# Performance work log

Hardware: AMD Instinct MI355X
Metric: run time of the kernel (lower is better)

The kernel has to match this reference:

```python
import jax, jax.numpy as jnp
import numpy as np

A = 5            # num_anchors
NC = 20          # num_classes
IGNORE_THRESH = 0.6
COORD_SCALE = 1.0
NOOBJ_SCALE = 1.0
OBJ_SCALE = 5.0
CLASS_SCALE = 1.0
ANCHORS_NP = np.array([[0.052, 0.066], [0.14, 0.11], [0.24, 0.30], [0.45, 0.42], [0.77, 0.72]], dtype=np.float32)


def setup_inputs() -> dict:
    key = jax.random.key(0)
    k1, k2, k3, k4, k5 = jax.random.split(key, 5)
    B, F, O = 32, 38, 50
    C = A * (5 + NC)
    outputs = jax.random.normal(k1, (B, C, F, F), jnp.float32)
    # targets: (cx, cy, w, h, cls) normalized; padded rows are all-zero
    cxy = jax.random.uniform(k2, (B, O, 2), minval=0.15, maxval=0.85)
    wh = jax.random.uniform(k3, (B, O, 2), minval=0.05, maxval=0.20)
    cls = jax.random.randint(k4, (B, O), 0, NC).astype(jnp.float32)
    targets = jnp.concatenate([cxy, wh, cls[..., None]], axis=-1)
    nobj = jax.random.randint(k5, (B,), 10, O + 1)
    valid = (jnp.arange(O)[None, :] < nobj[:, None]).astype(jnp.float32)
    targets = targets * valid[..., None]
    return {"outputs": outputs, "targets": targets, "anchors": jnp.asarray(ANCHORS_NP)}


def _pairwise_iou_xywh(a, b):
    # a: (..., N, 4), b: (..., M, 4) center-format -> IoU (..., N, M)
    a = a[..., :, None, :]
    b = b[..., None, :, :]
    tl = jnp.maximum(a[..., :2] - a[..., 2:] * 0.5, b[..., :2] - b[..., 2:] * 0.5)
    br = jnp.minimum(a[..., :2] + a[..., 2:] * 0.5, b[..., :2] + b[..., 2:] * 0.5)
    wh = jnp.clip(br - tl, 0.0)
    inter = wh[..., 0] * wh[..., 1]
    area_a = a[..., 2] * a[..., 3]
    area_b = b[..., 2] * b[..., 3]
    return inter / (area_a + area_b - inter + 1e-12)


def _forward(outputs, targets, anchors):
    B, C, F, _ = outputs.shape
    S = F * F
    O = targets.shape[1]
    valid = targets.sum(axis=2) > 0                    # (B, O)
    gt = targets[..., :4] * F                          # grid-unit cxywh
    gt_cls = targets[..., 4]

    out5 = outputs.reshape(B, A, 5 + NC, F, F)
    jj = jnp.arange(F, dtype=outputs.dtype)            # x (last axis)
    ii = jnp.arange(F, dtype=outputs.dtype)[:, None]   # y
    aw = (anchors[:, 0] * F)[None, :, None, None]
    ah = (anchors[:, 1] * F)[None, :, None, None]
    px = jax.nn.sigmoid(out5[:, :, 0]) + jj
    py = jax.nn.sigmoid(out5[:, :, 1]) + ii
    pw = jnp.exp(out5[:, :, 2]) * aw
    ph = jnp.exp(out5[:, :, 3]) * ah
    pred_boxes = jnp.stack([px, py, pw, ph], -1).transpose(0, 2, 3, 1, 4).reshape(B, S * A, 4)

    # anchor prior boxes at cell centers: (S, A, 4)
    ax = jnp.broadcast_to(jj + 0.5, (F, F))
    ay = jnp.broadcast_to(ii + 0.5, (F, F))
    aa = jnp.stack([
        jnp.broadcast_to(ax[:, :, None], (F, F, A)),
        jnp.broadcast_to(ay[:, :, None], (F, F, A)),
        jnp.broadcast_to((anchors[:, 0] * F)[None, None, :], (F, F, A)),
        jnp.broadcast_to((anchors[:, 1] * F)[None, None, :], (F, F, A)),
    ], -1).reshape(S, A, 4)

    ious = _pairwise_iou_xywh(pred_boxes, gt)          # (B, S*A, O)
    ious = jnp.where(valid[:, None, :], ious, 0.0)     # padded objs excluded (IoU >= 0)
    max_iou = ious.reshape(B, S, A, O).max(axis=-1)    # (B, S, A)

    n_pos = jnp.any(max_iou > IGNORE_THRESH, axis=(1, 2))
    iou_mask = jnp.full((B, S, A), NOOBJ_SCALE, outputs.dtype)
    iou_mask = jnp.where(n_pos[:, None, None] & (max_iou >= IGNORE_THRESH), 0.0, iou_mask)

    overlaps = _pairwise_iou_xywh(aa.reshape(1, S * A, 4), gt).reshape(B, S, A, O)

    # responsible cell: floor of top-left corner (faithful to source), anchor = argmax prior overlap
    x1y1 = gt[..., :2] - gt[..., 2:] * 0.5
    cxcy = jnp.floor(x1y1).astype(jnp.int32)
    cell = jnp.clip(cxcy[..., 1] * F + cxcy[..., 0], 0, S - 1)             # (B, O)
    ovT = overlaps.transpose(0, 3, 1, 2)                                   # (B, O, S, A)
    ov_cell = jnp.take_along_axis(ovT, cell[:, :, None, None], axis=2)[:, :, 0, :]
    anchor_idx = jnp.argmax(ov_cell, axis=-1)                              # (B, O)
    resp = aa[cell, anchor_idx]                                            # (B, O, 4)
    deltas = jnp.stack([gt[..., 0] - resp[..., 0], gt[..., 1] - resp[..., 1],
                        gt[..., 2] / resp[..., 2], gt[..., 3] / resp[..., 3]], -1)
    mi = jnp.take_along_axis(jnp.take_along_axis(max_iou, cell[:, :, None], axis=1),
                             anchor_idx[:, :, None], axis=2)[..., 0]       # (B, O)

    b_rep = jnp.broadcast_to(jnp.arange(B)[:, None], (B, O))
    cell_s = jnp.where(valid, cell, S)  # OOB index for padded objs -> dropped
    zt = jnp.zeros((B, S, A), outputs.dtype)
    box_target = jnp.zeros((B, S, A, 4), outputs.dtype).at[b_rep, cell_s, anchor_idx].set(deltas, mode='drop')
    box_mask = zt.at[b_rep, cell_s, anchor_idx].set(1.0, mode='drop')
    class_target = zt.at[b_rep, cell_s, anchor_idx].set(gt_cls, mode='drop')
    class_mask = zt.at[b_rep, cell_s, anchor_idx].set(1.0, mode='drop')
    iou_target = zt.at[b_rep, cell_s, anchor_idx].set(mi, mode='drop')
    iou_mask = iou_mask.at[b_rep, cell_s, anchor_idx].set(OBJ_SCALE, mode='drop')

    # prediction side, layout (B, (i*F+j)*A + a, 5+NC) matching target layout
    outs = out5.transpose(0, 3, 4, 1, 2).reshape(B, S * A, 5 + NC)
    pd = jnp.concatenate([jax.nn.sigmoid(outs[..., :2]), jnp.exp(outs[..., 2:4])], -1)
    conf = jax.nn.sigmoid(outs[..., 4])
    probs = jax.nn.softmax(outs[..., 5:], axis=-1)

    bm = box_mask.reshape(B, S * A, 1)
    im = iou_mask.reshape(B, S * A)
    box_loss = jnp.sum((pd * bm - box_target.reshape(B, S * A, 4) * bm) ** 2)
    iou_loss = jnp.sum((conf * im - iou_target.reshape(B, S * A) * im) ** 2)
    # faithful quirk of the source: cross-entropy applied to softmax *outputs* as logits
    ls = jax.nn.log_softmax(probs, axis=-1)
    ct = class_target.reshape(B, S * A).astype(jnp.int32)
    ce = -jnp.take_along_axis(ls, ct[..., None], axis=-1)[..., 0]
    class_loss = jnp.sum(ce * class_mask.reshape(B, S * A))
    return (COORD_SCALE * box_loss + iou_loss + CLASS_SCALE * class_loss) / B


def reference(outputs, targets, anchors):
    return _forward(outputs, targets, anchors)
```

## Files before the change

### kernel.cpp

```cpp
#include <hip/hip_runtime.h>
#include <math.h>

#define A_N 5
#define NC 20
#define FD 38
#define SD (FD*FD)
#define BD 32
#define OD 50
#define SA (SD*A_N)
#define HALF (SA/2)
#define GXP 15
#define SLOTB 16
#define NSLOT (BD * SLOTB)
#define IGN_T 0.6f
#define OBJ_S 5.0f

__device__ __forceinline__ float sigm(float x) { return 1.0f / (1.0f + __expf(-x)); }

__global__ __launch_bounds__(256) void k_main(
    const float* __restrict__ outputs, const float* __restrict__ targets,
    const float* __restrict__ anchors,
    float* __restrict__ pbase, float* __restrict__ pcorr, int* __restrict__ pflag)
{
    __shared__ float4 g_box[OD];
    __shared__ float  g_e[OD];
    __shared__ float  s_anc[2 * A_N];
    __shared__ int    s_cnt, s_any;
    __shared__ int    s_key[OD];
    __shared__ float  wb[4], wc[4];

    const int b = blockIdx.y;
    const int tid = threadIdx.x;
    if (tid == 0) s_any = 0;
    if (tid < 2 * A_N) s_anc[tid] = anchors[tid];

    if (blockIdx.x == GXP) {
        if (tid == 0) s_cnt = 0;
        __syncthreads();
        float gx = 0, gy = 0, gw = 0, gh = 0;
        int ct = 0, key = -1;
        if (tid < OD) {
            const float* t = targets + (b * OD + tid) * 5;
            float tx = t[0], ty = t[1], tw = t[2], th = t[3], tc = t[4];
            if (tx + ty + tw + th + tc > 0.0f) {
                gx = tx * FD; gy = ty * FD; gw = tw * FD; gh = th * FD;
                float gtlx = gx - gw*0.5f, gtly = gy - gh*0.5f;
                float gbrx = gx + gw*0.5f, gbry = gy + gh*0.5f;
                int k = atomicAdd(&s_cnt, 1);
                g_box[k] = make_float4(gtlx, gtly, gbrx, gbry);
                g_e[k] = gw * gh + 1e-12f;
                int cx = (int)floorf(gtlx), cy = (int)floorf(gtly);
                int cell = min(max(cy * FD + cx, 0), SD - 1);
                int ci = cell / FD, cj = cell - ci * FD;
                float acx = (float)cj + 0.5f, acy = (float)ci + 0.5f;
                float areaB = gw * gh;
                float best = -1.0f; int bi = 0;
                for (int a = 0; a < A_N; ++a) {
                    float aw = s_anc[2*a] * FD, ah = s_anc[2*a+1] * FD;
                    float w = fmaxf(fminf(acx + aw*0.5f, gbrx) - fmaxf(acx - aw*0.5f, gtlx), 0.0f);
                    float h = fmaxf(fminf(acy + ah*0.5f, gbry) - fmaxf(acy - ah*0.5f, gtly), 0.0f);
                    float inter = w * h;
                    float iou = inter / (aw*ah + areaB - inter + 1e-12f);
                    if (iou > best) { best = iou; bi = a; }
                }
                key = bi * SD + cell;
                ct = (int)tc;
            }
        }
        if (tid < OD) s_key[tid] = key;
        __syncthreads();
        const int cnt = s_cnt;

        float rbase = 0.0f, rcorr = 0.0f;
        if (tid < OD && key >= 0) {
            int win = -1;
            #pragma unroll 10
            for (int o = 0; o < OD; ++o) win = (s_key[o] == key) ? o : win;
            if (win == tid) {
                int a = key / SD, cell = key - a * SD;
                int ci = cell / FD, cj = cell - ci * FD;
                const float* ob = outputs + ((size_t)b * (A_N * 25) + a * 25) * SD + cell;
                float o0 = ob[0], o1 = ob[SD], o2 = ob[2*SD], o3 = ob[3*SD], o4 = ob[4*SD];
                float aw = s_anc[2*a] * FD, ah = s_anc[2*a+1] * FD;
                float px = sigm(o0) + (float)cj;
                float py = sigm(o1) + (float)ci;
                float ew = __expf(o2), eh = __expf(o3);
                float pw = ew * aw, ph = eh * ah;
                float tlx = px - pw*0.5f, tly = py - ph*0.5f;
                float brx = px + pw*0.5f, bry = py + ph*0.5f;
                float ar = pw * ph;
                float bn = 0.0f, bd = 1.0f;
                for (int o = 0; o < cnt; ++o) {
                    float4 bx = g_box[o];
                    float w = fmaxf(fminf(brx, bx.z) - fmaxf(tlx, bx.x), 0.0f);
                    float h = fmaxf(fminf(bry, bx.w) - fmaxf(tly, bx.y), 0.0f);
                    float in = w * h, de = ar + g_e[o] - in;
                    if (in * bd > bn * de) { bn = in; bd = de; }
                }
                float mi = bn / bd;
                float conf = sigm(o4);
                float d = conf - mi;
                rbase += OBJ_S * OBJ_S * d * d;
                float c2 = conf * conf;
                if (bn >= IGN_T * bd) rcorr -= c2;
                else                  rbase -= c2;
                float dx = gx - ((float)cj + 0.5f);
                float dy = gy - ((float)ci + 0.5f);
                float e0 = sigm(o0) - dx;
                float e1 = sigm(o1) - dy;
                float e2 = ew - gw / aw;
                float e3 = eh - gh / ah;
                rbase += e0*e0 + e1*e1 + e2*e2 + e3*e3;
                const float* cb = ob + 5 * SD;
                float xmax = -INFINITY;
                #pragma unroll
                for (int k = 0; k < NC; ++k) xmax = fmaxf(xmax, cb[k * SD]);
                float esum = 0.0f;
                #pragma unroll
                for (int k = 0; k < NC; ++k) esum += __expf(cb[k * SD] - xmax);
                float inv = 1.0f / esum;
                float pmax = inv;
                float pct = __expf(cb[ct * SD] - xmax) * inv;
                float e2s = 0.0f;
                #pragma unroll
                for (int k = 0; k < NC; ++k)
                    e2s += __expf(__expf(cb[k * SD] - xmax) * inv - pmax);
                rbase += -(pct - (pmax + __logf(e2s)));
            }
        }
        #pragma unroll
        for (int off = 32; off > 0; off >>= 1) {
            rbase += __shfl_down(rbase, off);
            rcorr += __shfl_down(rcorr, off);
        }
        int lane = tid & 63, w = tid >> 6;
        if (lane == 0) { wb[w] = rbase; wc[w] = rcorr; }
        __syncthreads();
        if (tid == 0) {
            int gid = b * SLOTB + GXP;
            pbase[gid] = wb[0] + wb[1] + wb[2] + wb[3];
            pcorr[gid] = wc[0] + wc[1] + wc[2] + wc[3];
            pflag[gid] = 0;
        }
        return;
    }

    const int ix = blockIdx.x * 256 + tid;
    const bool act = (ix < HALF);
    const int p0 = ix, p1 = ix + HALF;
    int a0 = p0 / SD, r0 = p0 - a0 * SD;
    int a1 = p1 / SD, r1 = p1 - a1 * SD;
    int ii0 = r0 / FD, jj0 = r0 - ii0 * FD;
    int ii1 = r1 / FD, jj1 = r1 - ii1 * FD;
    const float* ob0 = outputs + ((size_t)b * (A_N * 25) + a0 * 25) * SD + r0;
    const float* ob1 = outputs + ((size_t)b * (A_N * 25) + a1 * 25) * SD + r1;
    float q00 = 0, q01 = 0, q02 = 0, q03 = 0, q04 = 0;
    float q10 = 0, q11 = 0, q12 = 0, q13 = 0, q14 = 0;
    if (act) {
        q00 = ob0[0]; q01 = ob0[SD]; q02 = ob0[2*SD]; q03 = ob0[3*SD]; q04 = ob0[4*SD];
        q10 = ob1[0]; q11 = ob1[SD]; q12 = ob1[2*SD]; q13 = ob1[3*SD]; q14 = ob1[4*SD];
    }

    if (tid < 64) {
        bool v = false;
        float gtlx = 0, gtly = 0, gbrx = 0, gbry = 0, e = 0;
        if (tid < OD) {
            const float* t = targets + (b * OD + tid) * 5;
            float tx = t[0], ty = t[1], tw = t[2], th = t[3], tc = t[4];
            if (tx + ty + tw + th + tc > 0.0f) {
                v = true;
                float gx = tx * FD, gy = ty * FD, gw = tw * FD, gh = th * FD;
                gtlx = gx - gw*0.5f; gtly = gy - gh*0.5f;
                gbrx = gx + gw*0.5f; gbry = gy + gh*0.5f;
                e = IGN_T * (gw * gh + 1e-12f);
            }
        }
        unsigned long long bal = __ballot(v);
        if (v) {
            int k = __popcll(bal & ((1ull << tid) - 1ull));
            g_box[k] = make_float4(gtlx, gtly, gbrx, gbry);
            g_e[k] = e;
        }
        if (tid == 0) s_cnt = __popcll(bal);
    }
    __syncthreads();
    const int cnt = s_cnt;

    float base = 0.0f, corr = 0.0f;
    bool hot = false;
    if (act) {
        float aw0 = s_anc[2*a0] * FD, ah0 = s_anc[2*a0+1] * FD;
        float aw1 = s_anc[2*a1] * FD, ah1 = s_anc[2*a1+1] * FD;
        float px0 = sigm(q00) + (float)jj0, py0 = sigm(q01) + (float)ii0;
        float px1 = sigm(q10) + (float)jj1, py1 = sigm(q11) + (float)ii1;
        float pw0 = __expf(q02) * aw0, ph0 = __expf(q03) * ah0;
        float pw1 = __expf(q12) * aw1, ph1 = __expf(q13) * ah1;
        float tlx0 = px0 - pw0*0.5f, tly0 = py0 - ph0*0.5f;
        float brx0 = px0 + pw0*0.5f, bry0 = py0 + ph0*0.5f;
        float tlx1 = px1 - pw1*0.5f, tly1 = py1 - ph1*0.5f;
        float brx1 = px1 + pw1*0.5f, bry1 = py1 + ph1*0.5f;
        float f60 = IGN_T * (pw0 * ph0);
        float f61 = IGN_T * (pw1 * ph1);

        float dm0 = -1e30f, dm1 = -1e30f;
        for (int o = 0; o < cnt; ++o) {
            float4 bx = g_box[o];
            float e = g_e[o];
            float w0 = fmaxf(fminf(brx0, bx.z) - fmaxf(tlx0, bx.x), 0.0f);
            float h0 = fmaxf(fminf(bry0, bx.w) - fmaxf(tly0, bx.y), 0.0f);
            dm0 = fmaxf(dm0, fmaf((1.0f + IGN_T), w0 * h0, -(e + f60)));
            float w1 = fmaxf(fminf(brx1, bx.z) - fmaxf(tlx1, bx.x), 0.0f);
            float h1 = fmaxf(fminf(bry1, bx.w) - fmaxf(tly1, bx.y), 0.0f);
            dm1 = fmaxf(dm1, fmaf((1.0f + IGN_T), w1 * h1, -(e + f61)));
        }
        hot = (dm0 > 0.0f) || (dm1 > 0.0f);
        float c0 = sigm(q04); c0 *= c0;
        float c1 = sigm(q14); c1 *= c1;
        if (dm0 >= 0.0f) corr += c0; else base += c0;
        if (dm1 >= 0.0f) corr += c1; else base += c1;
    }

    unsigned long long bal = __ballot(hot);
    if ((tid & 63) == 0 && bal) atomicOr(&s_any, 1);

    #pragma unroll
    for (int off = 32; off > 0; off >>= 1) {
        base += __shfl_down(base, off);
        corr += __shfl_down(corr, off);
    }
    int lane = tid & 63, w = tid >> 6;
    if (lane == 0) { wb[w] = base; wc[w] = corr; }
    __syncthreads();
    if (tid == 0) {
        int gid = b * SLOTB + blockIdx.x;
        pbase[gid] = wb[0] + wb[1] + wb[2] + wb[3];
        pcorr[gid] = wc[0] + wc[1] + wc[2] + wc[3];
        pflag[gid] = s_any;
    }
}

__global__ __launch_bounds__(256) void k_fin(
    const float* __restrict__ pbase, const float* __restrict__ pcorr,
    const int* __restrict__ pflag, float* __restrict__ out)
{
    __shared__ int npos[BD];
    __shared__ float wsum[4];
    const int tid = threadIdx.x;
    if (tid < BD) {
        int f = 0;
        for (int x = 0; x < SLOTB; ++x) f |= pflag[tid * SLOTB + x];
        npos[tid] = f;
    }
    __syncthreads();
    float s = 0.0f;
    for (int g = tid; g < NSLOT; g += 256)
        s += pbase[g] + (npos[g >> 4] ? 0.0f : pcorr[g]);
    #pragma unroll
    for (int off = 32; off > 0; off >>= 1) s += __shfl_down(s, off);
    int lane = tid & 63, w = tid >> 6;
    if (lane == 0) wsum[w] = s;
    __syncthreads();
    if (tid == 0) out[0] = (wsum[0] + wsum[1] + wsum[2] + wsum[3]) * (1.0f / (float)BD);
}

extern "C" void kernel_launch(void* const* d_in, const int* in_sizes, int n_in,
                              void* d_out, int out_size, void* d_ws, size_t ws_size,
                              hipStream_t stream) {
    (void)in_sizes; (void)n_in; (void)out_size; (void)ws_size;
    const float* outputs = (const float*)d_in[0];
    const float* targets = (const float*)d_in[1];
    const float* anchors = (const float*)d_in[2];
    float* out = (float*)d_out;

    float* pbase = (float*)d_ws;
    float* pcorr = pbase + NSLOT;
    int*   pflag = (int*)(pcorr + NSLOT);

    k_main<<<dim3(GXP + 1, BD), 256, 0, stream>>>(outputs, targets, anchors,
                                                  pbase, pcorr, pflag);
    k_fin<<<dim3(1), 256, 0, stream>>>(pbase, pcorr, pflag, out);
}
```

Before: 77.26 us.

## Fuse per-image loss into one 1024-thread block and drop finalize kernel

Restructures the work so each image is handled by a single 1024-thread block that processes all anchor cells in chunks, computes the positive-target terms, and resolves the no-positive correction locally. The result is accumulated with a global atomicAdd after a memset, replacing the second reduction kernel and the workspace partials. This removes one kernel launch and the cross-block flag merge. The cost is far fewer blocks (32 instead of 512) on a many-CU GPU, so parallelism drops sharply, and atomic float accumulation makes the summation order nondeterministic.

```diff
diff --git a/kernel.cpp b/kernel.cpp
--- a/kernel.cpp
+++ b/kernel.cpp
@@ -8,47 +8,44 @@
 #define BD 32
 #define OD 50
 #define SA (SD*A_N)
-#define HALF (SA/2)
-#define GXP 15
-#define SLOTB 16
-#define NSLOT (BD * SLOTB)
+#define NT 1024
+#define CHUNK 4
 #define IGN_T 0.6f
 #define OBJ_S 5.0f
 
 __device__ __forceinline__ float sigm(float x) { return 1.0f / (1.0f + __expf(-x)); }
 
-__global__ __launch_bounds__(256) void k_main(
+__global__ __launch_bounds__(NT) void k_all(
     const float* __restrict__ outputs, const float* __restrict__ targets,
-    const float* __restrict__ anchors,
-    float* __restrict__ pbase, float* __restrict__ pcorr, int* __restrict__ pflag)
+    const float* __restrict__ anchors, float* __restrict__ out)
 {
     __shared__ float4 g_box[OD];
-    __shared__ float  g_e[OD];
+    __shared__ float  g_e6[OD];
+    __shared__ float  g_den[OD];
     __shared__ float  s_anc[2 * A_N];
+    __shared__ int    s_key[OD];
     __shared__ int    s_cnt, s_any;
-    __shared__ int    s_key[OD];
-    __shared__ float  wb[4], wc[4];
-
-    const int b = blockIdx.y;
+    __shared__ float  wb[NT/64], wc[NT/64];
+
+    const int b   = blockIdx.x;
     const int tid = threadIdx.x;
-    if (tid == 0) s_any = 0;
+    if (tid == 0) { s_any = 0; s_cnt = 0; }
     if (tid < 2 * A_N) s_anc[tid] = anchors[tid];
 
-    if (blockIdx.x == GXP) {
-        if (tid == 0) s_cnt = 0;
-        __syncthreads();
-        float gx = 0, gy = 0, gw = 0, gh = 0;
-        int ct = 0, key = -1;
+    float gx = 0, gy = 0, gw = 0, gh = 0;
+    int key = -1, ct = 0;
+    if (tid < 64) {
+        bool v = false;
+        float gtlx = 0, gtly = 0, gbrx = 0, gbry = 0, den = 0;
         if (tid < OD) {
             const float* t = targets + (b * OD + tid) * 5;
             float tx = t[0], ty = t[1], tw = t[2], th = t[3], tc = t[4];
             if (tx + ty + tw + th + tc > 0.0f) {
+                v = true;
                 gx = tx * FD; gy = ty * FD; gw = tw * FD; gh = th * FD;
-                float gtlx = gx - gw*0.5f, gtly = gy - gh*0.5f;
-                float gbrx = gx + gw*0.5f, gbry = gy + gh*0.5f;
-                int k = atomicAdd(&s_cnt, 1);
-                g_box[k] = make_float4(gtlx, gtly, gbrx, gbry);
-                g_e[k] = gw * gh + 1e-12f;
+                gtlx = gx - gw*0.5f; gtly = gy - gh*0.5f;
+                gbrx = gx + gw*0.5f; gbry = gy + gh*0.5f;
+                den  = gw * gh + 1e-12f;
                 int cx = (int)floorf(gtlx), cy = (int)floorf(gtly);
                 int cell = min(max(cy * FD + cx, 0), SD - 1);
                 int ci = cell / FD, cj = cell - ci * FD;
@@ -56,7 +53,7 @@
                 float areaB = gw * gh;
                 float best = -1.0f; int bi = 0;
                 for (int a = 0; a < A_N; ++a) {
-                    float aw = s_anc[2*a] * FD, ah = s_anc[2*a+1] * FD;
+                    float aw = anchors[2*a] * FD, ah = anchors[2*a+1] * FD;
                     float w = fmaxf(fminf(acx + aw*0.5f, gbrx) - fmaxf(acx - aw*0.5f, gtlx), 0.0f);
                     float h = fmaxf(fminf(acy + ah*0.5f, gbry) - fmaxf(acy - ah*0.5f, gtly), 0.0f);
                     float inter = w * h;
@@ -64,131 +61,95 @@
                     if (iou > best) { best = iou; bi = a; }
                 }
                 key = bi * SD + cell;
-                ct = (int)tc;
-            }
-        }
-        if (tid < OD) s_key[tid] = key;
-        __syncthreads();
-        const int cnt = s_cnt;
-
-        float rbase = 0.0f, rcorr = 0.0f;
-        if (tid < OD && key >= 0) {
-            int win = -1;
-            #pragma unroll 10
-            for (int o = 0; o < OD; ++o) win = (s_key[o] == key) ? o : win;
-            if (win == tid) {
-                int a = key / SD, cell = key - a * SD;
-                int ci = cell / FD, cj = cell - ci * FD;
-                const float* ob = outputs + ((size_t)b * (A_N * 25) + a * 25) * SD + cell;
-                float o0 = ob[0], o1 = ob[SD], o2 = ob[2*SD], o3 = ob[3*SD], o4 = ob[4*SD];
-                float aw = s_anc[2*a] * FD, ah = s_anc[2*a+1] * FD;
-                float px = sigm(o0) + (float)cj;
-                float py = sigm(o1) + (float)ci;
-                float ew = __expf(o2), eh = __expf(o3);
-                float pw = ew * aw, ph = eh * ah;
-                float tlx = px - pw*0.5f, tly = py - ph*0.5f;
-                float brx = px + pw*0.5f, bry = py + ph*0.5f;
-                float ar = pw * ph;
-                float bn = 0.0f, bd = 1.0f;
-                for (int o = 0; o < cnt; ++o) {
-                    float4 bx = g_box[o];
-                    float w = fmaxf(fminf(brx, bx.z) - fmaxf(tlx, bx.x), 0.0f);
-                    float h = fmaxf(fminf(bry, bx.w) - fmaxf(tly, bx.y), 0.0f);
-                    float in = w * h, de = ar + g_e[o] - in;
-                    if (in * bd > bn * de) { bn = in; bd = de; }
-                }
-                float mi = bn / bd;
-                float conf = sigm(o4);
-                float d = conf - mi;
-                rbase += OBJ_S * OBJ_S * d * d;
-                float c2 = conf * conf;
-                if (bn >= IGN_T * bd) rcorr -= c2;
-                else                  rbase -= c2;
-                float dx = gx - ((float)cj + 0.5f);
-                float dy = gy - ((float)ci + 0.5f);
-                float e0 = sigm(o0) - dx;
-                float e1 = sigm(o1) - dy;
-                float e2 = ew - gw / aw;
-                float e3 = eh - gh / ah;
-                rbase += e0*e0 + e1*e1 + e2*e2 + e3*e3;
-                const float* cb = ob + 5 * SD;
-                float xmax = -INFINITY;
-                #pragma unroll
-                for (int k = 0; k < NC; ++k) xmax = fmaxf(xmax, cb[k * SD]);
-                float esum = 0.0f;
-                #pragma unroll
-                for (int k = 0; k < NC; ++k) esum += __expf(cb[k * SD] - xmax);
-                float inv = 1.0f / esum;
-                float pmax = inv;
-                float pct = __expf(cb[ct * SD] - xmax) * inv;
-                float e2s = 0.0f;
-                #pragma unroll
-                for (int k = 0; k < NC; ++k)
-                    e2s += __expf(__expf(cb[k * SD] - xmax) * inv - pmax);
-                rbase += -(pct - (pmax + __logf(e2s)));
-            }
-        }
-        #pragma unroll
-        for (int off = 32; off > 0; off >>= 1) {
-            rbase += __shfl_down(rbase, off);
-            rcorr += __shfl_down(rcorr, off);
-        }
-        int lane = tid & 63, w = tid >> 6;
-        if (lane == 0) { wb[w] = rbase; wc[w] = rcorr; }
-        __syncthreads();
-        if (tid == 0) {
-            int gid = b * SLOTB + GXP;
-            pbase[gid] = wb[0] + wb[1] + wb[2] + wb[3];
-            pcorr[gid] = wc[0] + wc[1] + wc[2] + wc[3];
-            pflag[gid] = 0;
-        }
-        return;
-    }
-
-    const int ix = blockIdx.x * 256 + tid;
-    const bool act = (ix < HALF);
-    const int p0 = ix, p1 = ix + HALF;
-    int a0 = p0 / SD, r0 = p0 - a0 * SD;
-    int a1 = p1 / SD, r1 = p1 - a1 * SD;
-    int ii0 = r0 / FD, jj0 = r0 - ii0 * FD;
-    int ii1 = r1 / FD, jj1 = r1 - ii1 * FD;
-    const float* ob0 = outputs + ((size_t)b * (A_N * 25) + a0 * 25) * SD + r0;
-    const float* ob1 = outputs + ((size_t)b * (A_N * 25) + a1 * 25) * SD + r1;
-    float q00 = 0, q01 = 0, q02 = 0, q03 = 0, q04 = 0;
-    float q10 = 0, q11 = 0, q12 = 0, q13 = 0, q14 = 0;
-    if (act) {
-        q00 = ob0[0]; q01 = ob0[SD]; q02 = ob0[2*SD]; q03 = ob0[3*SD]; q04 = ob0[4*SD];
-        q10 = ob1[0]; q11 = ob1[SD]; q12 = ob1[2*SD]; q13 = ob1[3*SD]; q14 = ob1[4*SD];
-    }
-
-    if (tid < 64) {
-        bool v = false;
-        float gtlx = 0, gtly = 0, gbrx = 0, gbry = 0, e = 0;
-        if (tid < OD) {
-            const float* t = targets + (b * OD + tid) * 5;
-            float tx = t[0], ty = t[1], tw = t[2], th = t[3], tc = t[4];
-            if (tx + ty + tw + th + tc > 0.0f) {
-                v = true;
-                float gx = tx * FD, gy = ty * FD, gw = tw * FD, gh = th * FD;
-                gtlx = gx - gw*0.5f; gtly = gy - gh*0.5f;
-                gbrx = gx + gw*0.5f; gbry = gy + gh*0.5f;
-                e = IGN_T * (gw * gh + 1e-12f);
+                ct  = (int)tc;
             }
         }
         unsigned long long bal = __ballot(v);
         if (v) {
             int k = __popcll(bal & ((1ull << tid) - 1ull));
             g_box[k] = make_float4(gtlx, gtly, gbrx, gbry);
-            g_e[k] = e;
+            g_e6[k]  = IGN_T * den;
+            g_den[k] = den;
         }
         if (tid == 0) s_cnt = __popcll(bal);
+        if (tid < OD) s_key[tid] = key;
     }
     __syncthreads();
     const int cnt = s_cnt;
 
     float base = 0.0f, corr = 0.0f;
-    bool hot = false;
-    if (act) {
+    bool  hot  = false;
+
+    if (tid < OD && key >= 0) {
+        int win = -1;
+        #pragma unroll 10
+        for (int o = 0; o < OD; ++o) win = (s_key[o] == key) ? o : win;
+        if (win == tid) {
+            int a = key / SD, cell = key - a * SD;
+            int ci = cell / FD, cj = cell - ci * FD;
+            const float* ob = outputs + ((size_t)b * (A_N * 25) + a * 25) * SD + cell;
+            float o0 = ob[0], o1 = ob[SD], o2 = ob[2*SD], o3 = ob[3*SD], o4 = ob[4*SD];
+            float aw = s_anc[2*a] * FD, ah = s_anc[2*a+1] * FD;
+            float px = sigm(o0) + (float)cj;
+            float py = sigm(o1) + (float)ci;
+            float ew = __expf(o2), eh = __expf(o3);
+            float pw = ew * aw, ph = eh * ah;
+            float tlx = px - pw*0.5f, tly = py - ph*0.5f;
+            float brx = px + pw*0.5f, bry = py + ph*0.5f;
+            float ar = pw * ph;
+            float bn = 0.0f, bd = 1.0f;
+            for (int o = 0; o < cnt; ++o) {
+                float4 bx = g_box[o];
+                float w = fmaxf(fminf(brx, bx.z) - fmaxf(tlx, bx.x), 0.0f);
+                float h = fmaxf(fminf(bry, bx.w) - fmaxf(tly, bx.y), 0.0f);
+                float in = w * h, de = ar + g_den[o] - in;
+                if (in * bd > bn * de) { bn = in; bd = de; }
+            }
+            float mi = bn / bd;
+            float conf = sigm(o4);
+            float d = conf - mi;
+            base += OBJ_S * OBJ_S * d * d;
+            float c2 = conf * conf;
+            if (bn >= IGN_T * bd) corr -= c2;
+            else                  base -= c2;
+            float dx = gx - ((float)cj + 0.5f);
+            float dy = gy - ((float)ci + 0.5f);
+            float e0 = sigm(o0) - dx;
+            float e1 = sigm(o1) - dy;
+            float e2 = ew - gw / aw;
+            float e3 = eh - gh / ah;
+            base += e0*e0 + e1*e1 + e2*e2 + e3*e3;
+            const float* cb = ob + 5 * SD;
+            float xmax = -INFINITY;
+            #pragma unroll
+            for (int k = 0; k < NC; ++k) xmax = fmaxf(xmax, cb[k * SD]);
+            float esum = 0.0f;
+            #pragma unroll
+            for (int k = 0; k < NC; ++k) esum += __expf(cb[k * SD] - xmax);
+            float inv = 1.0f / esum;
+            float pmax = inv;
+            float pct = __expf(cb[ct * SD] - xmax) * inv;
+            float e2s = 0.0f;
+            #pragma unroll
+            for (int k = 0; k < NC; ++k)
+                e2s += __expf(__expf(cb[k * SD] - xmax) * inv - pmax);
+            base += -(pct - (pmax + __logf(e2s)));
+        }
+    }
+
+    for (int c = 0; c < CHUNK; ++c) {
+        const int p0 = c * NT + tid;
+        const bool act1 = (p0 + CHUNK * NT < SA);
+        const int p1 = act1 ? (p0 + CHUNK * NT) : (SA - 1);
+        int a0 = p0 / SD, r0 = p0 - a0 * SD;
+        int a1 = p1 / SD, r1 = p1 - a1 * SD;
+        int ii0 = r0 / FD, jj0 = r0 - ii0 * FD;
+        int ii1 = r1 / FD, jj1 = r1 - ii1 * FD;
+        const float* ob0 = outputs + ((size_t)b * (A_N * 25) + a0 * 25) * SD + r0;
+        const float* ob1 = outputs + ((size_t)b * (A_N * 25) + a1 * 25) * SD + r1;
+        float q00 = ob0[0], q01 = ob0[SD], q02 = ob0[2*SD], q03 = ob0[3*SD], q04 = ob0[4*SD];
+        float q10 = ob1[0], q11 = ob1[SD], q12 = ob1[2*SD], q13 = ob1[3*SD], q14 = ob1[4*SD];
+
         float aw0 = s_anc[2*a0] * FD, ah0 = s_anc[2*a0+1] * FD;
         float aw1 = s_anc[2*a1] * FD, ah1 = s_anc[2*a1+1] * FD;
         float px0 = sigm(q00) + (float)jj0, py0 = sigm(q01) + (float)ii0;
@@ -205,7 +166,7 @@
         float dm0 = -1e30f, dm1 = -1e30f;
         for (int o = 0; o < cnt; ++o) {
             float4 bx = g_box[o];
-            float e = g_e[o];
+            float e = g_e6[o];
             float w0 = fmaxf(fminf(brx0, bx.z) - fmaxf(tlx0, bx.x), 0.0f);
             float h0 = fmaxf(fminf(bry0, bx.w) - fmaxf(tly0, bx.y), 0.0f);
             dm0 = fmaxf(dm0, fmaf((1.0f + IGN_T), w0 * h0, -(e + f60)));
@@ -213,70 +174,39 @@
             float h1 = fmaxf(fminf(bry1, bx.w) - fmaxf(tly1, bx.y), 0.0f);
             dm1 = fmaxf(dm1, fmaf((1.0f + IGN_T), w1 * h1, -(e + f61)));
         }
-        hot = (dm0 > 0.0f) || (dm1 > 0.0f);
         float c0 = sigm(q04); c0 *= c0;
         float c1 = sigm(q14); c1 *= c1;
+        hot = hot || (dm0 > 0.0f) || (act1 && (dm1 > 0.0f));
         if (dm0 >= 0.0f) corr += c0; else base += c0;
-        if (dm1 >= 0.0f) corr += c1; else base += c1;
-    }
-
-    unsigned long long bal = __ballot(hot);
-    if ((tid & 63) == 0 && bal) atomicOr(&s_any, 1);
-
+        if (act1) { if (dm1 >= 0.0f) corr += c1; else base += c1; }
+    }
+
+    unsigned long long hb = __ballot(hot);
+    if ((tid & 63) == 0 && hb) atomicOr(&s_any, 1);
     #pragma unroll
     for (int off = 32; off > 0; off >>= 1) {
         base += __shfl_down(base, off);
         corr += __shfl_down(corr, off);
     }
-    int lane = tid & 63, w = tid >> 6;
-    if (lane == 0) { wb[w] = base; wc[w] = corr; }
+    const int lane = tid & 63, wv = tid >> 6;
+    if (lane == 0) { wb[wv] = base; wc[wv] = corr; }
     __syncthreads();
     if (tid == 0) {
-        int gid = b * SLOTB + blockIdx.x;
-        pbase[gid] = wb[0] + wb[1] + wb[2] + wb[3];
-        pcorr[gid] = wc[0] + wc[1] + wc[2] + wc[3];
-        pflag[gid] = s_any;
-    }
-}
-
-__global__ __launch_bounds__(256) void k_fin(
-    const float* __restrict__ pbase, const float* __restrict__ pcorr,
-    const int* __restrict__ pflag, float* __restrict__ out)
-{
-    __shared__ int npos[BD];
-    __shared__ float wsum[4];
-    const int tid = threadIdx.x;
-    if (tid < BD) {
-        int f = 0;
-        for (int x = 0; x < SLOTB; ++x) f |= pflag[tid * SLOTB + x];
-        npos[tid] = f;
-    }
-    __syncthreads();
-    float s = 0.0f;
-    for (int g = tid; g < NSLOT; g += 256)
-        s += pbase[g] + (npos[g >> 4] ? 0.0f : pcorr[g]);
-    #pragma unroll
-    for (int off = 32; off > 0; off >>= 1) s += __shfl_down(s, off);
-    int lane = tid & 63, w = tid >> 6;
-    if (lane == 0) wsum[w] = s;
-    __syncthreads();
-    if (tid == 0) out[0] = (wsum[0] + wsum[1] + wsum[2] + wsum[3]) * (1.0f / (float)BD);
+        float sb = 0.0f, sc = 0.0f;
+        #pragma unroll
+        for (int i = 0; i < NT/64; ++i) { sb += wb[i]; sc += wc[i]; }
+        float contrib = sb + (s_any ? 0.0f : sc);
+        atomicAdd(out, contrib * (1.0f / (float)BD));
+    }
 }
 
 extern "C" void kernel_launch(void* const* d_in, const int* in_sizes, int n_in,
                               void* d_out, int out_size, void* d_ws, size_t ws_size,
                               hipStream_t stream) {
-    (void)in_sizes; (void)n_in; (void)out_size; (void)ws_size;
-    const float* outputs = (const float*)d_in[0];
-    const float* targets = (const float*)d_in[1];
-    const float* anchors = (const float*)d_in[2];
-    float* out = (float*)d_out;
-
-    float* pbase = (float*)d_ws;
-    float* pcorr = pbase + NSLOT;
-    int*   pflag = (int*)(pcorr + NSLOT);
-
-    k_main<<<dim3(GXP + 1, BD), 256, 0, stream>>>(outputs, targets, anchors,
-                                                  pbase, pcorr, pflag);
-    k_fin<<<dim3(1), 256, 0, stream>>>(pbase, pcorr, pflag, out);
+    (void)in_sizes; (void)n_in; (void)out_size; (void)d_ws; (void)ws_size;
+    hipMemsetAsync(d_out, 0, sizeof(float), stream);
+    k_all<<<dim3(BD), NT, 0, stream>>>((const float*)d_in[0],
+                                       (const float*)d_in[1],
+                                       (const float*)d_in[2],
+                                       (float*)d_out);
 }
```

New measurement: 112.4 us. +45.4%, slower.
